# Performance work log

Hardware: AMD Instinct MI355X
Metric: run time of the kernel (lower is better)

Reference implementation:

```python
import jax, jax.numpy as jnp
import numpy as np
import math

H = 1024
E = 16
ENT_STRENGTH = 0.5
COHERENCE_TIME = 10.0
TIME_STEP = 0.0
K = 2
# static list of rotation pairs (i<j), applied sequentially as in the torch double loop
PAIRS = np.array([(i, j) for i in range(E) for j in range(i + 1, E)], dtype=np.int32)


def _mlp(x, w1, b1, w2, b2):
    h = jax.nn.gelu(x @ w1 + b1, approximate=False)  # torch default GELU = exact erf
    return h @ w2 + b2


def _apply_entanglement(amps, ent):
    # sequential Givens rotations over expert pairs; carry shape [B,S,E]
    pairs = jnp.asarray(PAIRS)

    def step(carry, pair):
        i, j = pair[0], pair[1]
        angle = ent[i, j] * ENT_STRENGTH
        c, s = jnp.cos(angle), jnp.sin(angle)
        ai = jnp.take(carry, i, axis=-1)  # [B,S]
        aj = jnp.take(carry, j, axis=-1)
        oh_i = jax.nn.one_hot(i, E, dtype=carry.dtype)
        oh_j = jax.nn.one_hot(j, E, dtype=carry.dtype)
        new = (carry * (1.0 - oh_i - oh_j)
               + (c * ai - s * aj)[..., None] * oh_i
               + (s * ai + c * aj)[..., None] * oh_j)
        return new, None

    out, _ = jax.lax.scan(step, amps, pairs)
    return out


def setup_inputs() -> dict:
    key = jax.random.key(0)
    ks = jax.random.split(key, 10)
    sc1 = 1.0 / math.sqrt(H)
    sc2 = 1.0 / math.sqrt(H // 2)
    return {
        "hidden_states": jax.random.normal(ks[0], (4, 4096, H), dtype=jnp.float32),
        "w1a": jax.random.uniform(ks[1], (H, H // 2), jnp.float32, -sc1, sc1),
        "b1a": jnp.zeros((H // 2,), jnp.float32),
        "w2a": jax.random.uniform(ks[2], (H // 2, E), jnp.float32, -sc2, sc2),
        "b2a": jnp.zeros((E,), jnp.float32),
        "w1p": jax.random.uniform(ks[3], (H, H // 2), jnp.float32, -sc1, sc1),
        "b1p": jnp.zeros((H // 2,), jnp.float32),
        "w2p": jax.random.uniform(ks[4], (H // 2, E), jnp.float32, -sc2, sc2),
        "b2p": jnp.zeros((E,), jnp.float32),
        "ent": jax.random.normal(ks[5], (E, E), dtype=jnp.float32) * 0.1,
    }


def reference(hidden_states, w1a, b1a, w2a, b2a, w1p, b1p, w2p, b2p, ent):
    raw_amps = _mlp(hidden_states, w1a, b1a, w2a, b2a)                 # [B,S,E]
    raw_phases = jnp.tanh(_mlp(hidden_states, w1p, b1p, w2p, b2p)) * jnp.float32(math.pi)
    amplitudes = jnp.sqrt(jax.nn.softmax(jnp.abs(raw_amps), axis=-1))
    entangled = _apply_entanglement(amplitudes, ent)
    coherence = jnp.exp(jnp.float32(-TIME_STEP / COHERENCE_TIME))      # time_step buffer = 0 -> 1.0
    decoherent = entangled * coherence
    probs = decoherent ** 2
    probs = probs / jnp.maximum(jnp.sum(jnp.abs(probs), axis=-1, keepdims=True), 1e-12)
    top_p, top_i = jax.lax.top_k(probs, K)
    top_p = top_p / jnp.maximum(jnp.sum(jnp.abs(top_p), axis=-1, keepdims=True), 1e-12)
    return top_p, top_i, decoherent, raw_phases, probs
```

## Files before the change

### kernel.cpp

```cpp
#include <hip/hip_runtime.h>
#include <math.h>

#define NTOK   16384
#define HDIM   1024
#define HHALF  512
#define NE     16

#define OFF_TP  0
#define OFF_TI  (NTOK * 2)
#define OFF_DEC (NTOK * 4)
#define OFF_PH  (OFF_DEC + NTOK * NE)
#define OFF_PR  (OFF_PH + NTOK * NE)

typedef _Float16 half8 __attribute__((ext_vector_type(8)));
typedef _Float16 half4 __attribute__((ext_vector_type(4)));
typedef float f32x16 __attribute__((ext_vector_type(16)));
typedef float f32x4 __attribute__((ext_vector_type(4)));

#define LO_SCALE     2048.0f
#define LO_SCALE_INV (1.0f / 2048.0f)
#define MFMA32(a,b,c) __builtin_amdgcn_mfma_f32_32x32x16_f16(a,b,c,0,0,0)
#define MFMA16(a,b,c) __builtin_amdgcn_mfma_f32_16x16x32_f16(a,b,c,0,0,0)

#define BAR() asm volatile("s_waitcnt lgkmcnt(0)\n\ts_barrier" ::: "memory")

__device__ __forceinline__ float gelu_exact(float x) {
    return 0.5f * x * (1.0f + erff(x * 0.70710678118654752440f));
}

__device__ __forceinline__ void cvt_split(float4 v, half4& hi, half4& lo) {
    _Float16 h0 = (_Float16)v.x, h1 = (_Float16)v.y,
             h2 = (_Float16)v.z, h3 = (_Float16)v.w;
    hi = (half4){h0, h1, h2, h3};
    lo = (half4){(_Float16)((v.x - (float)h0) * LO_SCALE),
                 (_Float16)((v.y - (float)h1) * LO_SCALE),
                 (_Float16)((v.z - (float)h2) * LO_SCALE),
                 (_Float16)((v.w - (float)h3) * LO_SCALE)};
}

__global__ void __launch_bounds__(256)
qir_wtrans(const float* __restrict__ w1a, const float* __restrict__ w1p,
           _Float16* __restrict__ wt, float* __restrict__ out)
{
    int u = blockIdx.x * 256 + threadIdx.x;
    out[OFF_PH + u] = 0.0f;
    out[OFF_PH + 262144 + u] = 0.0f;

    int l  = u & 63;
    int f  = (u >> 6) & 7;
    int sl = (u >> 9) & 7;
    int kc = (u >> 12) & 31;
    int ph = u >> 17;
    int nf = f >> 2, kh = (f >> 1) & 1, pl = f & 1;
    int col = sl * 64 + nf * 32 + (l & 31);
    int k0  = kc * 32 + kh * 16 + (l >> 5) * 8;
    const float* __restrict__ W = ph ? w1p : w1a;
    half8 v;
    #pragma unroll
    for (int j = 0; j < 8; ++j) {
        float x = W[(size_t)(k0 + j) * HHALF + col];
        _Float16 h = (_Float16)x;
        v[j] = pl ? (_Float16)((x - (float)h) * LO_SCALE) : h;
    }
    *(half8*)&wt[(size_t)u * 8] = v;
}

__device__ __forceinline__ void kstep(
    int kc, const float* __restrict__ aptr, const _Float16* __restrict__ bptr,
    char* Acur, char* Anxt, int a_rd, int a_off0, int a_off1,
    half8 (&Bc)[8], half8 (&Bn)[8],
    float4 (&xw)[2], float4 (&xl)[2],
    f32x16& a00, f32x16& a01, f32x16& a10, f32x16& a11,
    f32x16& c00, f32x16& c01, f32x16& c10, f32x16& c11)
{
    if (kc + 2 < 32) {
        xl[0] = *(const float4*)(aptr + (kc + 2) * 32);
        xl[1] = *(const float4*)(aptr + (kc + 2) * 32 + 16);
    }
    if (kc + 1 < 32) {
        #pragma unroll
        for (int f = 0; f < 8; ++f)
            Bn[f] = *(const half8*)(bptr + (size_t)(kc + 1) * 32768 + f * 512);
    }
    #pragma unroll
    for (int kh = 0; kh < 2; ++kh) {
        const char* Ah = Acur + kh * 4096 + a_rd;
        half8 ah0 = *(const half8*)(Ah);
        half8 ah1 = *(const half8*)(Ah + 512);
        half8 al0 = *(const half8*)(Ah + 8192);
        half8 al1 = *(const half8*)(Ah + 8192 + 512);
        half8 bh0 = Bc[kh * 2],     bl0 = Bc[kh * 2 + 1];
        half8 bh1 = Bc[4 + kh * 2], bl1 = Bc[4 + kh * 2 + 1];
        a00 = MFMA32(ah0, bh0, a00); c00 = MFMA32(al0, bh0, c00); c00 = MFMA32(ah0, bl0, c00);
        a01 = MFMA32(ah0, bh1, a01); c01 = MFMA32(al0, bh1, c01); c01 = MFMA32(ah0, bl1, c01);
        a10 = MFMA32(ah1, bh0, a10); c10 = MFMA32(al1, bh0, c10); c10 = MFMA32(ah1, bl0, c10);
        a11 = MFMA32(ah1, bh1, a11); c11 = MFMA32(al1, bh1, c11); c11 = MFMA32(ah1, bl1, c11);
    }
    if (kc + 1 < 32) {
        half4 hv, lv;
        cvt_split(xw[0], hv, lv);
        *(half4*)(Anxt + a_off0) = hv; *(half4*)(Anxt + a_off0 + 8192) = lv;
        cvt_split(xw[1], hv, lv);
        *(half4*)(Anxt + a_off1) = hv; *(half4*)(Anxt + a_off1 + 8192) = lv;
    }
    BAR();
}

__global__ void __launch_bounds__(512, 2)
qir_gemm(const float* __restrict__ xg, const _Float16* __restrict__ wt,
         const float* __restrict__ b1a, const float* __restrict__ w2a, const float* __restrict__ b2a,
         const float* __restrict__ b1p, const float* __restrict__ w2p, const float* __restrict__ b2p,
         float* __restrict__ out)
{
    extern __shared__ char smem[];
    const int tid = threadIdx.x;
    const int l  = tid & 63;
    const int w  = tid >> 6;
    const int wm = w >> 2;
    const int wn = w & 3;
    const int bid  = blockIdx.x;
    const int mblk = bid & 127;
    const int v    = bid >> 7;
    const int ph   = v & 1;
    const int nh   = v >> 1;
    const int tok0 = mblk * 128;

    const float* __restrict__ b1 = ph ? b1p : b1a;
    const float* __restrict__ w2 = ph ? w2p : w2a;
    const float* __restrict__ b2 = ph ? b2p : b2a;
    const _Float16* __restrict__ wtp = wt + ((size_t)ph << 20);

    char* const Ab0 = smem;
    char* const Ab1 = smem + 16384;

    const int r  = tid >> 2;
    const int kq = tid & 3;
    const float* __restrict__ aptr = xg + (size_t)(tok0 + r) * HDIM + kq * 4;
    const int a_off0 = (kq >> 1) * 2048 + r * 16 + (kq & 1) * 8;
    const int a_off1 = a_off0 + 4096;
    const int a_rd = (l >> 5) * 2048 + (wm * 64 + (l & 31)) * 16;

    const _Float16* __restrict__ bptr = wtp + (nh * 4 + wn) * 4096 + (size_t)l * 8;

    f32x16 a00{}, a01{}, a10{}, a11{}, c00{}, c01{}, c10{}, c11{};
    #pragma unroll
    for (int rg = 0; rg < 16; ++rg) {
        a00[rg] = 0.f; a01[rg] = 0.f; a10[rg] = 0.f; a11[rg] = 0.f;
        c00[rg] = 0.f; c01[rg] = 0.f; c10[rg] = 0.f; c11[rg] = 0.f;
    }

    half8 Bc[8], Bn[8];
    float4 xw[2], xl[2];

    {
        float4 v0 = *(const float4*)(aptr);
        float4 v1 = *(const float4*)(aptr + 16);
        half4 hv, lv;
        cvt_split(v0, hv, lv);
        *(half4*)(Ab0 + a_off0) = hv; *(half4*)(Ab0 + a_off0 + 8192) = lv;
        cvt_split(v1, hv, lv);
        *(half4*)(Ab0 + a_off1) = hv; *(half4*)(Ab0 + a_off1 + 8192) = lv;
    }
    #pragma unroll
    for (int f = 0; f < 8; ++f) Bc[f] = *(const half8*)(bptr + f * 512);
    xw[0] = *(const float4*)(aptr + 32);
    xw[1] = *(const float4*)(aptr + 48);
    BAR();

    for (int kk = 0; kk < 16; ++kk) {
        kstep(2 * kk,     aptr, bptr, Ab0, Ab1, a_rd, a_off0, a_off1,
              Bc, Bn, xw, xl, a00, a01, a10, a11, c00, c01, c10, c11);
        kstep(2 * kk + 1, aptr, bptr, Ab1, Ab0, a_rd, a_off0, a_off1,
              Bn, Bc, xl, xw, a00, a01, a10, a11, c00, c01, c10, c11);
    }

    const int col0 = nh * 256 + wn * 64 + (l & 31);
    const float bb0 = b1[col0], bb1 = b1[col0 + 32];
    #pragma unroll
    for (int rg = 0; rg < 16; ++rg) {
        a00[rg] = gelu_exact(a00[rg] + c00[rg] * LO_SCALE_INV + bb0);
        a01[rg] = gelu_exact(a01[rg] + c01[rg] * LO_SCALE_INV + bb1);
        a10[rg] = gelu_exact(a10[rg] + c10[rg] * LO_SCALE_INV + bb0);
        a11[rg] = gelu_exact(a11[rg] + c11[rg] * LO_SCALE_INV + bb1);
    }

    char* const Hw = smem + w * 4096;
    char* const hb = Hw + ((l >> 3) & 3) * 1024 + (l & 7) * 2;
    float* const P = (float*)(smem + 32768);

    half8 w2h[2], w2l[2];
    #pragma unroll
    for (int nf = 0; nf < 2; ++nf) {
        #pragma unroll
        for (int j = 0; j < 8; ++j) {
            int kg = nh * 256 + wn * 64 + nf * 32 + (l >> 4) * 8 + j;
            float vv = w2[(size_t)kg * NE + (l & 15)];
            _Float16 hh = (_Float16)vv;
            w2h[nf][j] = hh;
            w2l[nf][j] = (_Float16)((vv - (float)hh) * LO_SCALE);
        }
    }

    f32x4 acc2[4], acc2s[4];
    #pragma unroll
    for (int m16 = 0; m16 < 4; ++m16)
        #pragma unroll
        for (int rg = 0; rg < 4; ++rg) { acc2[m16][rg] = 0.f; acc2s[m16][rg] = 0.f; }

#define H2PASS(ACC0, ACC1, NF, PL)                                             \
    {                                                                          \
        _Pragma("unroll")                                                      \
        for (int rg = 0; rg < 16; ++rg) {                                      \
            int row0 = (rg & 3) + 8 * (rg >> 2) + 4 * (l >> 5);                \
            { float vv = ACC0[rg]; _Float16 hh = (_Float16)vv;                 \
              *(_Float16*)(hb + row0 * 16) =                                   \
                  (PL) ? (_Float16)(vv - (float)hh) : hh; }                    \
            { float vv = ACC1[rg]; _Float16 hh = (_Float16)vv;                 \
              *(_Float16*)(hb + (32 + row0) * 16) =                            \
                  (PL) ? (_Float16)(vv - (float)hh) : hh; }                    \
        }                                                                      \
        _Pragma("unroll")                                                      \
        for (int m16 = 0; m16 < 4; ++m16) {                                    \
            half8 a2 = *(const half8*)(Hw + (l >> 4) * 1024 +                  \
                                       (m16 * 16 + (l & 15)) * 16);            \
            acc2[m16] = MFMA16(a2, w2h[NF], acc2[m16]);                        \
            if (!(PL)) acc2s[m16] = MFMA16(a2, w2l[NF], acc2s[m16]);           \
        }                                                                      \
    }

    H2PASS(a00, a10, 0, 0)
    H2PASS(a01, a11, 1, 0)
    H2PASS(a00, a10, 0, 1)
    H2PASS(a01, a11, 1, 1)
#undef H2PASS

    #pragma unroll
    for (int m16 = 0; m16 < 4; ++m16)
        #pragma unroll
        for (int rg = 0; rg < 4; ++rg) {
            int row = m16 * 16 + ((l >> 4) << 2) + rg;
            P[w * 1024 + row * 16 + (l & 15)] =
                acc2[m16][rg] + acc2s[m16][rg] * LO_SCALE_INV;
        }
    __syncthreads();

    #pragma unroll
    for (int rep = 0; rep < 4; ++rep) {
        int oi = tid + rep * 512;
        int t = oi >> 4, e = oi & 15;
        int bw = (t >> 6) * 4, tl = t & 63;
        float sum = 0.5f * b2[e]
                  + P[(bw + 0) * 1024 + tl * 16 + e]
                  + P[(bw + 1) * 1024 + tl * 16 + e]
                  + P[(bw + 2) * 1024 + tl * 16 + e]
                  + P[(bw + 3) * 1024 + tl * 16 + e];
        atomicAdd(out + (ph ? OFF_PH : OFF_PR) + (size_t)(tok0 + t) * NE + e, sum);
    }
}

__global__ void __launch_bounds__(512)
qir_mlp(const float* __restrict__ xg,
        const float* __restrict__ w1a, const float* __restrict__ b1a,
        const float* __restrict__ w2a, const float* __restrict__ b2a,
        const float* __restrict__ w1p, const float* __restrict__ b1p,
        const float* __restrict__ w2p, const float* __restrict__ b2p,
        float* __restrict__ out)
{
    __shared__ float sh_w[16][HHALF];
    __shared__ float sh_x[16][68];

    const int tid  = threadIdx.x;
    const int cg   = tid & 63;
    const int tg   = tid >> 6;
    const int tok0 = blockIdx.x * 64;
    const int cA   = cg * 4;
    const int cB   = 256 + cg * 4;

    for (int phase = 0; phase < 2; ++phase) {
        const float* __restrict__ w1 = phase ? w1p : w1a;
        const float* __restrict__ b1 = phase ? b1p : b1a;
        const float* __restrict__ w2 = phase ? w2p : w2a;
        const float* __restrict__ b2 = phase ? b2p : b2a;

        float acc[8][8];
        #pragma unroll
        for (int t = 0; t < 8; ++t)
            #pragma unroll
            for (int c = 0; c < 8; ++c) acc[t][c] = 0.0f;

        float4 wreg[4];
        float4 xreg = make_float4(0.f, 0.f, 0.f, 0.f);

        auto load_chunk = [&](int kc) {
            #pragma unroll
            for (int p = 0; p < 4; ++p) {
                int f  = tid + p * 512;
                int k  = f >> 7;
                int c4 = (f & 127) << 2;
                wreg[p] = *(const float4*)&w1[(kc * 16 + k) * HHALF + c4];
            }
            if (tid < 256) {
                int t  = tid >> 2;
                int k4 = (tid & 3) << 2;
                xreg = *(const float4*)&xg[(size_t)(tok0 + t) * HDIM + kc * 16 + k4];
            }
        };

        load_chunk(0);
        for (int kc = 0; kc < HDIM / 16; ++kc) {
            __syncthreads();
            #pragma unroll
            for (int p = 0; p < 4; ++p) {
                int f  = tid + p * 512;
                int k  = f >> 7;
                int c4 = (f & 127) << 2;
                *(float4*)&sh_w[k][c4] = wreg[p];
            }
            if (tid < 256) {
                int t  = tid >> 2;
                int k4 = (tid & 3) << 2;
                sh_x[k4 + 0][t] = xreg.x;
                sh_x[k4 + 1][t] = xreg.y;
                sh_x[k4 + 2][t] = xreg.z;
                sh_x[k4 + 3][t] = xreg.w;
            }
            __syncthreads();
            if (kc + 1 < HDIM / 16) load_chunk(kc + 1);

            #pragma unroll 4
            for (int k = 0; k < 16; ++k) {
                float4 xa = *(const float4*)&sh_x[k][tg * 8];
                float4 xb = *(const float4*)&sh_x[k][tg * 8 + 4];
                float4 wa = *(const float4*)&sh_w[k][cA];
                float4 wb = *(const float4*)&sh_w[k][cB];
                float xs[8] = {xa.x, xa.y, xa.z, xa.w, xb.x, xb.y, xb.z, xb.w};
                float ws[8] = {wa.x, wa.y, wa.z, wa.w, wb.x, wb.y, wb.z, wb.w};
                #pragma unroll
                for (int t = 0; t < 8; ++t)
                    #pragma unroll
                    for (int c = 0; c < 8; ++c)
                        acc[t][c] = fmaf(xs[t], ws[c], acc[t][c]);
            }
        }

        {
            float4 bA4 = *(const float4*)&b1[cA];
            float4 bB4 = *(const float4*)&b1[cB];
            float bs[8] = {bA4.x, bA4.y, bA4.z, bA4.w, bB4.x, bB4.y, bB4.z, bB4.w};
            #pragma unroll
            for (int t = 0; t < 8; ++t)
                #pragma unroll
                for (int c = 0; c < 8; ++c)
                    acc[t][c] = gelu_exact(acc[t][c] + bs[c]);
        }

        for (int e = 0; e < NE; ++e) {
            float w2v[8];
            #pragma unroll
            for (int j = 0; j < 4; ++j) {
                w2v[j]     = w2[(cA + j) * NE + e];
                w2v[4 + j] = w2[(cB + j) * NE + e];
            }
            float bias2 = b2[e];
            #pragma unroll
            for (int t = 0; t < 8; ++t) {
                float s = 0.0f;
                #pragma unroll
                for (int j = 0; j < 8; ++j) s = fmaf(acc[t][j], w2v[j], s);
                #pragma unroll
                for (int off = 1; off < 64; off <<= 1)
                    s += __shfl_xor(s, off, 64);
                if (cg == 0) {
                    float raw   = s + bias2;
                    int   token = tok0 + tg * 8 + t;
                    out[(phase ? OFF_PH : OFF_PR) + (size_t)token * NE + e] = raw;
                }
            }
        }
    }
}

__global__ void __launch_bounds__(256)
qir_epilogue(const float* __restrict__ ent, float* __restrict__ out)
{
    __shared__ float sh_c[120], sh_s[120];
    const int tid = threadIdx.x;
    if (tid < 120) {
        int rem = tid, i = 0;
        while (rem >= 15 - i) { rem -= 15 - i; ++i; }
        int j = i + 1 + rem;
        float ang = ent[i * NE + j] * 0.5f;
        sh_c[tid] = cosf(ang);
        sh_s[tid] = sinf(ang);
    }
    __syncthreads();

    const int token = blockIdx.x * 256 + tid;

    #pragma unroll
    for (int q = 0; q < 4; ++q) {
        float4 v = *(const float4*)&out[OFF_PH + (size_t)token * NE + q * 4];
        v.x = tanhf(v.x) * 3.14159265358979323846f;
        v.y = tanhf(v.y) * 3.14159265358979323846f;
        v.z = tanhf(v.z) * 3.14159265358979323846f;
        v.w = tanhf(v.w) * 3.14159265358979323846f;
        *(float4*)&out[OFF_PH + (size_t)token * NE + q * 4] = v;
    }

    float a[16];
    #pragma unroll
    for (int q = 0; q < 4; ++q) {
        float4 v = *(const float4*)&out[OFF_PR + (size_t)token * NE + q * 4];
        a[q*4+0] = v.x; a[q*4+1] = v.y; a[q*4+2] = v.z; a[q*4+3] = v.w;
    }

    float m = fabsf(a[0]);
    #pragma unroll
    for (int e = 1; e < 16; ++e) m = fmaxf(m, fabsf(a[e]));
    float ssum = 0.0f;
    #pragma unroll
    for (int e = 0; e < 16; ++e) { a[e] = expf(fabsf(a[e]) - m); ssum += a[e]; }
    float inv = 1.0f / ssum;
    #pragma unroll
    for (int e = 0; e < 16; ++e) a[e] = sqrtf(a[e] * inv);

    {
        int p = 0;
        #pragma unroll
        for (int i = 0; i < 16; ++i) {
            #pragma unroll
            for (int j = i + 1; j < 16; ++j) {
                float c = sh_c[p], s = sh_s[p]; ++p;
                float ai = a[i], aj = a[j];
                a[i] = c * ai - s * aj;
                a[j] = s * ai + c * aj;
            }
        }
    }

    #pragma unroll
    for (int q = 0; q < 4; ++q)
        *(float4*)&out[OFF_DEC + (size_t)token * NE + q * 4] =
            make_float4(a[q*4], a[q*4+1], a[q*4+2], a[q*4+3]);

    float pr[16];
    float s2 = 0.0f;
    #pragma unroll
    for (int e = 0; e < 16; ++e) { pr[e] = a[e] * a[e]; s2 += pr[e]; }
    float inv2 = 1.0f / fmaxf(s2, 1e-12f);
    #pragma unroll
    for (int e = 0; e < 16; ++e) pr[e] *= inv2;
    #pragma unroll
    for (int q = 0; q < 4; ++q)
        *(float4*)&out[OFF_PR + (size_t)token * NE + q * 4] =
            make_float4(pr[q*4], pr[q*4+1], pr[q*4+2], pr[q*4+3]);

    float bv = pr[0]; int bi = 0;
    #pragma unroll
    for (int e = 1; e < 16; ++e) if (pr[e] > bv) { bv = pr[e]; bi = e; }
    float sv = -1.0f; int si = 0;
    #pragma unroll
    for (int e = 0; e < 16; ++e) if (e != bi && pr[e] > sv) { sv = pr[e]; si = e; }
    float ts = fmaxf(fabsf(bv) + fabsf(sv), 1e-12f);
    out[OFF_TP + (size_t)token * 2 + 0] = bv / ts;
    out[OFF_TP + (size_t)token * 2 + 1] = sv / ts;
    out[OFF_TI + (size_t)token * 2 + 0] = (float)bi;
    out[OFF_TI + (size_t)token * 2 + 1] = (float)si;
}

extern "C" void kernel_launch(void* const* d_in, const int* in_sizes, int n_in,
                              void* d_out, int out_size, void* d_ws, size_t ws_size,
                              hipStream_t stream) {
    const float* xg  = (const float*)d_in[0];
    const float* w1a = (const float*)d_in[1];
    const float* b1a = (const float*)d_in[2];
    const float* w2a = (const float*)d_in[3];
    const float* b2a = (const float*)d_in[4];
    const float* w1p = (const float*)d_in[5];
    const float* b1p = (const float*)d_in[6];
    const float* w2p = (const float*)d_in[7];
    const float* b2p = (const float*)d_in[8];
    const float* ent = (const float*)d_in[9];
    float* out = (float*)d_out;

    if (ws_size >= (size_t)4 * 1024 * 1024) {
        _Float16* wt = (_Float16*)d_ws;
        qir_wtrans<<<1024, 256, 0, stream>>>(w1a, w1p, wt, out);
        qir_gemm<<<512, 512, 65536, stream>>>(xg, wt, b1a, w2a, b2a,
                                              b1p, w2p, b2p, out);
    } else {
        qir_mlp<<<NTOK / 64, 512, 0, stream>>>(xg, w1a, b1a, w2a, b2a,
                                               w1p, b1p, w2p, b2p, out);
    }
    qir_epilogue<<<NTOK / 256, 256, 0, stream>>>(ent, out);
}
```

Baseline: 131.7 us.

## Remap GEMM warps to 128x32 strips sharing B fragments across four M tiles

Changes the per-wave tile of the first GEMM from 64x64 (2x2 of 32x32 MFMA tiles) to 128x32 (4x1), so each wave loads half as much B weight data per k-step but reads twice as much A from LDS. The second-layer projection is reorganized to match: hidden activations are staged per wave in padded LDS rows, and partial sums from all 8 waves are reduced instead of 4. This trades global B traffic and registers for more LDS reads and a larger cross-wave reduction.

```diff
diff --git a/kernel.cpp b/kernel.cpp
--- a/kernel.cpp
+++ b/kernel.cpp
@@ -68,10 +68,9 @@
 __device__ __forceinline__ void kstep(
     int kc, const float* __restrict__ aptr, const _Float16* __restrict__ bptr,
     char* Acur, char* Anxt, int a_rd, int a_off0, int a_off1,
-    half8 (&Bc)[8], half8 (&Bn)[8],
+    half8 (&Bc)[4], half8 (&Bn)[4],
     float4 (&xw)[2], float4 (&xl)[2],
-    f32x16& a00, f32x16& a01, f32x16& a10, f32x16& a11,
-    f32x16& c00, f32x16& c01, f32x16& c10, f32x16& c11)
+    f32x16 (&am)[4], f32x16 (&cm)[4])
 {
     if (kc + 2 < 32) {
         xl[0] = *(const float4*)(aptr + (kc + 2) * 32);
@@ -79,22 +78,25 @@
     }
     if (kc + 1 < 32) {
         #pragma unroll
-        for (int f = 0; f < 8; ++f)
-            Bn[f] = *(const half8*)(bptr + (size_t)(kc + 1) * 32768 + f * 512);
+        for (int j = 0; j < 4; ++j)
+            Bn[j] = *(const half8*)(bptr + (size_t)(kc + 1) * 32768 + j * 512);
     }
     #pragma unroll
     for (int kh = 0; kh < 2; ++kh) {
         const char* Ah = Acur + kh * 4096 + a_rd;
-        half8 ah0 = *(const half8*)(Ah);
-        half8 ah1 = *(const half8*)(Ah + 512);
-        half8 al0 = *(const half8*)(Ah + 8192);
-        half8 al1 = *(const half8*)(Ah + 8192 + 512);
-        half8 bh0 = Bc[kh * 2],     bl0 = Bc[kh * 2 + 1];
-        half8 bh1 = Bc[4 + kh * 2], bl1 = Bc[4 + kh * 2 + 1];
-        a00 = MFMA32(ah0, bh0, a00); c00 = MFMA32(al0, bh0, c00); c00 = MFMA32(ah0, bl0, c00);
-        a01 = MFMA32(ah0, bh1, a01); c01 = MFMA32(al0, bh1, c01); c01 = MFMA32(ah0, bl1, c01);
-        a10 = MFMA32(ah1, bh0, a10); c10 = MFMA32(al1, bh0, c10); c10 = MFMA32(ah1, bl0, c10);
-        a11 = MFMA32(ah1, bh1, a11); c11 = MFMA32(al1, bh1, c11); c11 = MFMA32(ah1, bl1, c11);
+        half8 ah[4], al[4];
+        #pragma unroll
+        for (int mf = 0; mf < 4; ++mf) {
+            ah[mf] = *(const half8*)(Ah + mf * 512);
+            al[mf] = *(const half8*)(Ah + 8192 + mf * 512);
+        }
+        half8 bh = Bc[kh * 2], bl = Bc[kh * 2 + 1];
+        #pragma unroll
+        for (int mf = 0; mf < 4; ++mf) {
+            am[mf] = MFMA32(ah[mf], bh, am[mf]);
+            cm[mf] = MFMA32(al[mf], bh, cm[mf]);
+            cm[mf] = MFMA32(ah[mf], bl, cm[mf]);
+        }
     }
     if (kc + 1 < 32) {
         half4 hv, lv;
@@ -116,8 +118,6 @@
     const int tid = threadIdx.x;
     const int l  = tid & 63;
     const int w  = tid >> 6;
-    const int wm = w >> 2;
-    const int wn = w & 3;
     const int bid  = blockIdx.x;
     const int mblk = bid & 127;
     const int v    = bid >> 7;
@@ -138,18 +138,19 @@
     const float* __restrict__ aptr = xg + (size_t)(tok0 + r) * HDIM + kq * 4;
     const int a_off0 = (kq >> 1) * 2048 + r * 16 + (kq & 1) * 8;
     const int a_off1 = a_off0 + 4096;
-    const int a_rd = (l >> 5) * 2048 + (wm * 64 + (l & 31)) * 16;
-
-    const _Float16* __restrict__ bptr = wtp + (nh * 4 + wn) * 4096 + (size_t)l * 8;
-
-    f32x16 a00{}, a01{}, a10{}, a11{}, c00{}, c01{}, c10{}, c11{};
-    #pragma unroll
-    for (int rg = 0; rg < 16; ++rg) {
-        a00[rg] = 0.f; a01[rg] = 0.f; a10[rg] = 0.f; a11[rg] = 0.f;
-        c00[rg] = 0.f; c01[rg] = 0.f; c10[rg] = 0.f; c11[rg] = 0.f;
-    }
-
-    half8 Bc[8], Bn[8];
+    const int a_rd = (l >> 5) * 2048 + (l & 31) * 16;
+
+    const int c32 = nh * 8 + w;
+    const _Float16* __restrict__ bptr =
+        wtp + (c32 >> 1) * 4096 + (c32 & 1) * 2048 + (size_t)l * 8;
+
+    f32x16 am[4], cm[4];
+    #pragma unroll
+    for (int mf = 0; mf < 4; ++mf)
+        #pragma unroll
+        for (int rg = 0; rg < 16; ++rg) { am[mf][rg] = 0.f; cm[mf][rg] = 0.f; }
+
+    half8 Bc[4], Bn[4];
     float4 xw[2], xl[2];
 
     {
@@ -162,98 +163,98 @@
         *(half4*)(Ab0 + a_off1) = hv; *(half4*)(Ab0 + a_off1 + 8192) = lv;
     }
     #pragma unroll
-    for (int f = 0; f < 8; ++f) Bc[f] = *(const half8*)(bptr + f * 512);
+    for (int j = 0; j < 4; ++j) Bc[j] = *(const half8*)(bptr + j * 512);
     xw[0] = *(const float4*)(aptr + 32);
     xw[1] = *(const float4*)(aptr + 48);
     BAR();
 
     for (int kk = 0; kk < 16; ++kk) {
         kstep(2 * kk,     aptr, bptr, Ab0, Ab1, a_rd, a_off0, a_off1,
-              Bc, Bn, xw, xl, a00, a01, a10, a11, c00, c01, c10, c11);
+              Bc, Bn, xw, xl, am, cm);
         kstep(2 * kk + 1, aptr, bptr, Ab1, Ab0, a_rd, a_off0, a_off1,
-              Bn, Bc, xl, xw, a00, a01, a10, a11, c00, c01, c10, c11);
-    }
-
-    const int col0 = nh * 256 + wn * 64 + (l & 31);
-    const float bb0 = b1[col0], bb1 = b1[col0 + 32];
-    #pragma unroll
-    for (int rg = 0; rg < 16; ++rg) {
-        a00[rg] = gelu_exact(a00[rg] + c00[rg] * LO_SCALE_INV + bb0);
-        a01[rg] = gelu_exact(a01[rg] + c01[rg] * LO_SCALE_INV + bb1);
-        a10[rg] = gelu_exact(a10[rg] + c10[rg] * LO_SCALE_INV + bb0);
-        a11[rg] = gelu_exact(a11[rg] + c11[rg] * LO_SCALE_INV + bb1);
-    }
-
-    char* const Hw = smem + w * 4096;
-    char* const hb = Hw + ((l >> 3) & 3) * 1024 + (l & 7) * 2;
-    float* const P = (float*)(smem + 32768);
-
-    half8 w2h[2], w2l[2];
-    #pragma unroll
-    for (int nf = 0; nf < 2; ++nf) {
-        #pragma unroll
-        for (int j = 0; j < 8; ++j) {
-            int kg = nh * 256 + wn * 64 + nf * 32 + (l >> 4) * 8 + j;
-            float vv = w2[(size_t)kg * NE + (l & 15)];
-            _Float16 hh = (_Float16)vv;
-            w2h[nf][j] = hh;
-            w2l[nf][j] = (_Float16)((vv - (float)hh) * LO_SCALE);
-        }
-    }
-
-    f32x4 acc2[4], acc2s[4];
-    #pragma unroll
-    for (int m16 = 0; m16 < 4; ++m16)
-        #pragma unroll
-        for (int rg = 0; rg < 4; ++rg) { acc2[m16][rg] = 0.f; acc2s[m16][rg] = 0.f; }
-
-#define H2PASS(ACC0, ACC1, NF, PL)                                             \
-    {                                                                          \
-        _Pragma("unroll")                                                      \
-        for (int rg = 0; rg < 16; ++rg) {                                      \
-            int row0 = (rg & 3) + 8 * (rg >> 2) + 4 * (l >> 5);                \
-            { float vv = ACC0[rg]; _Float16 hh = (_Float16)vv;                 \
-              *(_Float16*)(hb + row0 * 16) =                                   \
-                  (PL) ? (_Float16)(vv - (float)hh) : hh; }                    \
-            { float vv = ACC1[rg]; _Float16 hh = (_Float16)vv;                 \
-              *(_Float16*)(hb + (32 + row0) * 16) =                            \
-                  (PL) ? (_Float16)(vv - (float)hh) : hh; }                    \
-        }                                                                      \
-        _Pragma("unroll")                                                      \
-        for (int m16 = 0; m16 < 4; ++m16) {                                    \
-            half8 a2 = *(const half8*)(Hw + (l >> 4) * 1024 +                  \
-                                       (m16 * 16 + (l & 15)) * 16);            \
-            acc2[m16] = MFMA16(a2, w2h[NF], acc2[m16]);                        \
-            if (!(PL)) acc2s[m16] = MFMA16(a2, w2l[NF], acc2s[m16]);           \
-        }                                                                      \
-    }
-
-    H2PASS(a00, a10, 0, 0)
-    H2PASS(a01, a11, 1, 0)
-    H2PASS(a00, a10, 0, 1)
-    H2PASS(a01, a11, 1, 1)
-#undef H2PASS
-
-    #pragma unroll
-    for (int m16 = 0; m16 < 4; ++m16)
-        #pragma unroll
-        for (int rg = 0; rg < 4; ++rg) {
-            int row = m16 * 16 + ((l >> 4) << 2) + rg;
-            P[w * 1024 + row * 16 + (l & 15)] =
-                acc2[m16][rg] + acc2s[m16][rg] * LO_SCALE_INV;
-        }
+              Bn, Bc, xl, xw, am, cm);
+    }
+
+    const float bb = b1[nh * 256 + w * 32 + (l & 31)];
+    #pragma unroll
+    for (int mf = 0; mf < 4; ++mf)
+        #pragma unroll
+        for (int rg = 0; rg < 16; ++rg)
+            am[mf][rg] = gelu_exact(am[mf][rg] + cm[mf][rg] * LO_SCALE_INV + bb);
+
+    char* const Hw = smem + w * 5120;
+
+    half8 w2h, w2l;
+    #pragma unroll
+    for (int j = 0; j < 8; ++j) {
+        int kg = nh * 256 + w * 32 + (l >> 4) * 8 + j;
+        float vv = w2[(size_t)kg * NE + (l & 15)];
+        _Float16 hh = (_Float16)vv;
+        w2h[j] = hh;
+        w2l[j] = (_Float16)((vv - (float)hh) * LO_SCALE);
+    }
+
+    f32x4 acc2[2][4], acc2s[2][4];
+    #pragma unroll
+    for (int p2 = 0; p2 < 2; ++p2)
+        #pragma unroll
+        for (int m16 = 0; m16 < 4; ++m16)
+            #pragma unroll
+            for (int rg = 0; rg < 4; ++rg) { acc2[p2][m16][rg] = 0.f; acc2s[p2][m16][rg] = 0.f; }
+
+    #pragma unroll
+    for (int p2 = 0; p2 < 2; ++p2) {
+        #pragma unroll
+        for (int fr = 0; fr < 2; ++fr)
+            #pragma unroll
+            for (int rg = 0; rg < 16; ++rg) {
+                int row = fr * 32 + (rg & 3) + 8 * (rg >> 2) + 4 * (l >> 5);
+                float vv = am[p2 * 2 + fr][rg];
+                *(_Float16*)(Hw + row * 80 + (l & 31) * 2) = (_Float16)vv;
+            }
+        #pragma unroll
+        for (int m16 = 0; m16 < 4; ++m16) {
+            half8 a2 = *(const half8*)(Hw + (m16 * 16 + (l & 15)) * 80 + (l >> 4) * 16);
+            acc2[p2][m16]  = MFMA16(a2, w2h, acc2[p2][m16]);
+            acc2s[p2][m16] = MFMA16(a2, w2l, acc2s[p2][m16]);
+        }
+        #pragma unroll
+        for (int fr = 0; fr < 2; ++fr)
+            #pragma unroll
+            for (int rg = 0; rg < 16; ++rg) {
+                int row = fr * 32 + (rg & 3) + 8 * (rg >> 2) + 4 * (l >> 5);
+                float vv = am[p2 * 2 + fr][rg];
+                _Float16 hh = (_Float16)vv;
+                *(_Float16*)(Hw + row * 80 + (l & 31) * 2) = (_Float16)(vv - (float)hh);
+            }
+        #pragma unroll
+        for (int m16 = 0; m16 < 4; ++m16) {
+            half8 a2 = *(const half8*)(Hw + (m16 * 16 + (l & 15)) * 80 + (l >> 4) * 16);
+            acc2[p2][m16] = MFMA16(a2, w2h, acc2[p2][m16]);
+        }
+    }
+
+    __syncthreads();
+    float* const P = (float*)smem;
+    #pragma unroll
+    for (int p2 = 0; p2 < 2; ++p2)
+        #pragma unroll
+        for (int m16 = 0; m16 < 4; ++m16)
+            #pragma unroll
+            for (int rg = 0; rg < 4; ++rg) {
+                int t = p2 * 64 + m16 * 16 + ((l >> 4) << 2) + rg;
+                P[w * 2048 + t * 16 + (l & 15)] =
+                    acc2[p2][m16][rg] + acc2s[p2][m16][rg] * LO_SCALE_INV;
+            }
     __syncthreads();
 
     #pragma unroll
     for (int rep = 0; rep < 4; ++rep) {
         int oi = tid + rep * 512;
         int t = oi >> 4, e = oi & 15;
-        int bw = (t >> 6) * 4, tl = t & 63;
-        float sum = 0.5f * b2[e]
-                  + P[(bw + 0) * 1024 + tl * 16 + e]
-                  + P[(bw + 1) * 1024 + tl * 16 + e]
-                  + P[(bw + 2) * 1024 + tl * 16 + e]
-                  + P[(bw + 3) * 1024 + tl * 16 + e];
+        float sum = 0.5f * b2[e];
+        #pragma unroll
+        for (int w8 = 0; w8 < 8; ++w8) sum += P[w8 * 2048 + t * 16 + e];
         atomicAdd(out + (ph ? OFF_PH : OFF_PR) + (size_t)(tok0 + t) * NE + e, sum);
     }
 }
```

Result: faster. 120.8 us (-8.3%).

## Process two K-chunks per barrier with larger LDS double buffer

Applied to the files above, without the earlier changes.

Restructures the main GEMM K loop so that each iteration stages a 64-wide K slab of the activations in LDS instead of a 32-wide one. This halves the number of block-wide barriers. The B fragments for the second half-slab are prefetched into a separate register set, and the next slab's B loads are issued in the middle of the MFMA sequence to overlap global latency with compute. In exchange, the A double buffer grows to 64 KB of LDS and the register footprint rises. The LDS growth could limit the two-blocks-per-CU occupancy and needs a matching dynamic shared-memory size at launch.

```diff
diff --git a/kernel.cpp b/kernel.cpp
--- a/kernel.cpp
+++ b/kernel.cpp
@@ -63,47 +63,6 @@
         v[j] = pl ? (_Float16)((x - (float)h) * LO_SCALE) : h;
     }
     *(half8*)&wt[(size_t)u * 8] = v;
-}
-
-__device__ __forceinline__ void kstep(
-    int kc, const float* __restrict__ aptr, const _Float16* __restrict__ bptr,
-    char* Acur, char* Anxt, int a_rd, int a_off0, int a_off1,
-    half8 (&Bc)[8], half8 (&Bn)[8],
-    float4 (&xw)[2], float4 (&xl)[2],
-    f32x16& a00, f32x16& a01, f32x16& a10, f32x16& a11,
-    f32x16& c00, f32x16& c01, f32x16& c10, f32x16& c11)
-{
-    if (kc + 2 < 32) {
-        xl[0] = *(const float4*)(aptr + (kc + 2) * 32);
-        xl[1] = *(const float4*)(aptr + (kc + 2) * 32 + 16);
-    }
-    if (kc + 1 < 32) {
-        #pragma unroll
-        for (int f = 0; f < 8; ++f)
-            Bn[f] = *(const half8*)(bptr + (size_t)(kc + 1) * 32768 + f * 512);
-    }
-    #pragma unroll
-    for (int kh = 0; kh < 2; ++kh) {
-        const char* Ah = Acur + kh * 4096 + a_rd;
-        half8 ah0 = *(const half8*)(Ah);
-        half8 ah1 = *(const half8*)(Ah + 512);
-        half8 al0 = *(const half8*)(Ah + 8192);
-        half8 al1 = *(const half8*)(Ah + 8192 + 512);
-        half8 bh0 = Bc[kh * 2],     bl0 = Bc[kh * 2 + 1];
-        half8 bh1 = Bc[4 + kh * 2], bl1 = Bc[4 + kh * 2 + 1];
-        a00 = MFMA32(ah0, bh0, a00); c00 = MFMA32(al0, bh0, c00); c00 = MFMA32(ah0, bl0, c00);
-        a01 = MFMA32(ah0, bh1, a01); c01 = MFMA32(al0, bh1, c01); c01 = MFMA32(ah0, bl1, c01);
-        a10 = MFMA32(ah1, bh0, a10); c10 = MFMA32(al1, bh0, c10); c10 = MFMA32(ah1, bl0, c10);
-        a11 = MFMA32(ah1, bh1, a11); c11 = MFMA32(al1, bh1, c11); c11 = MFMA32(ah1, bl1, c11);
-    }
-    if (kc + 1 < 32) {
-        half4 hv, lv;
-        cvt_split(xw[0], hv, lv);
-        *(half4*)(Anxt + a_off0) = hv; *(half4*)(Anxt + a_off0 + 8192) = lv;
-        cvt_split(xw[1], hv, lv);
-        *(half4*)(Anxt + a_off1) = hv; *(half4*)(Anxt + a_off1 + 8192) = lv;
-    }
-    BAR();
 }
 
 __global__ void __launch_bounds__(512, 2)
@@ -130,14 +89,10 @@
     const float* __restrict__ b2 = ph ? b2p : b2a;
     const _Float16* __restrict__ wtp = wt + ((size_t)ph << 20);
 
-    char* const Ab0 = smem;
-    char* const Ab1 = smem + 16384;
-
     const int r  = tid >> 2;
     const int kq = tid & 3;
     const float* __restrict__ aptr = xg + (size_t)(tok0 + r) * HDIM + kq * 4;
-    const int a_off0 = (kq >> 1) * 2048 + r * 16 + (kq & 1) * 8;
-    const int a_off1 = a_off0 + 4096;
+    const int a_woff = (kq >> 1) * 2048 + r * 16 + (kq & 1) * 8;
     const int a_rd = (l >> 5) * 2048 + (wm * 64 + (l & 31)) * 16;
 
     const _Float16* __restrict__ bptr = wtp + (nh * 4 + wn) * 4096 + (size_t)l * 8;
@@ -149,29 +104,84 @@
         c00[rg] = 0.f; c01[rg] = 0.f; c10[rg] = 0.f; c11[rg] = 0.f;
     }
 
-    half8 Bc[8], Bn[8];
-    float4 xw[2], xl[2];
+    half8 Bc[8], Bd[8];
+    float4 xw[4];
 
     {
-        float4 v0 = *(const float4*)(aptr);
-        float4 v1 = *(const float4*)(aptr + 16);
-        half4 hv, lv;
-        cvt_split(v0, hv, lv);
-        *(half4*)(Ab0 + a_off0) = hv; *(half4*)(Ab0 + a_off0 + 8192) = lv;
-        cvt_split(v1, hv, lv);
-        *(half4*)(Ab0 + a_off1) = hv; *(half4*)(Ab0 + a_off1 + 8192) = lv;
+        #pragma unroll
+        for (int c = 0; c < 4; ++c) {
+            float4 vv = *(const float4*)(aptr + c * 16);
+            half4 hv, lv;
+            cvt_split(vv, hv, lv);
+            *(half4*)(smem + a_woff + c * 4096) = hv;
+            *(half4*)(smem + a_woff + c * 4096 + 16384) = lv;
+        }
     }
     #pragma unroll
     for (int f = 0; f < 8; ++f) Bc[f] = *(const half8*)(bptr + f * 512);
-    xw[0] = *(const float4*)(aptr + 32);
-    xw[1] = *(const float4*)(aptr + 48);
     BAR();
 
-    for (int kk = 0; kk < 16; ++kk) {
-        kstep(2 * kk,     aptr, bptr, Ab0, Ab1, a_rd, a_off0, a_off1,
-              Bc, Bn, xw, xl, a00, a01, a10, a11, c00, c01, c10, c11);
-        kstep(2 * kk + 1, aptr, bptr, Ab1, Ab0, a_rd, a_off0, a_off1,
-              Bn, Bc, xl, xw, a00, a01, a10, a11, c00, c01, c10, c11);
+    #pragma unroll 1
+    for (int p = 0; p < 16; ++p) {
+        char* const cur = smem + (p & 1) * 32768;
+        char* const nxt = smem + ((p & 1) ^ 1) * 32768;
+
+        #pragma unroll
+        for (int f = 0; f < 8; ++f)
+            Bd[f] = *(const half8*)(bptr + (size_t)(2 * p + 1) * 32768 + f * 512);
+        if (p + 1 < 16) {
+            #pragma unroll
+            for (int c = 0; c < 4; ++c)
+                xw[c] = *(const float4*)(aptr + (p + 1) * 64 + c * 16);
+        }
+
+        #pragma unroll
+        for (int j = 0; j < 2; ++j) {
+            const char* Aj = cur + j * 4096 + a_rd;
+            half8 ah0 = *(const half8*)(Aj);
+            half8 ah1 = *(const half8*)(Aj + 512);
+            half8 al0 = *(const half8*)(Aj + 16384);
+            half8 al1 = *(const half8*)(Aj + 16384 + 512);
+            half8 bh0 = Bc[j * 2],     bl0 = Bc[j * 2 + 1];
+            half8 bh1 = Bc[4 + j * 2], bl1 = Bc[4 + j * 2 + 1];
+            a00 = MFMA32(ah0, bh0, a00); c00 = MFMA32(al0, bh0, c00); c00 = MFMA32(ah0, bl0, c00);
+            a01 = MFMA32(ah0, bh1, a01); c01 = MFMA32(al0, bh1, c01); c01 = MFMA32(ah0, bl1, c01);
+            a10 = MFMA32(ah1, bh0, a10); c10 = MFMA32(al1, bh0, c10); c10 = MFMA32(ah1, bl0, c10);
+            a11 = MFMA32(ah1, bh1, a11); c11 = MFMA32(al1, bh1, c11); c11 = MFMA32(ah1, bl1, c11);
+        }
+
+        if (p + 1 < 16) {
+            #pragma unroll
+            for (int f = 0; f < 8; ++f)
+                Bc[f] = *(const half8*)(bptr + (size_t)(2 * p + 2) * 32768 + f * 512);
+        }
+
+        #pragma unroll
+        for (int j = 2; j < 4; ++j) {
+            const char* Aj = cur + j * 4096 + a_rd;
+            half8 ah0 = *(const half8*)(Aj);
+            half8 ah1 = *(const half8*)(Aj + 512);
+            half8 al0 = *(const half8*)(Aj + 16384);
+            half8 al1 = *(const half8*)(Aj + 16384 + 512);
+            const int kh = j - 2;
+            half8 bh0 = Bd[kh * 2],     bl0 = Bd[kh * 2 + 1];
+            half8 bh1 = Bd[4 + kh * 2], bl1 = Bd[4 + kh * 2 + 1];
+            a00 = MFMA32(ah0, bh0, a00); c00 = MFMA32(al0, bh0, c00); c00 = MFMA32(ah0, bl0, c00);
+            a01 = MFMA32(ah0, bh1, a01); c01 = MFMA32(al0, bh1, c01); c01 = MFMA32(ah0, bl1, c01);
+            a10 = MFMA32(ah1, bh0, a10); c10 = MFMA32(al1, bh0, c10); c10 = MFMA32(ah1, bl0, c10);
+            a11 = MFMA32(ah1, bh1, a11); c11 = MFMA32(al1, bh1, c11); c11 = MFMA32(ah1, bl1, c11);
+        }
+
+        if (p + 1 < 16) {
+            #pragma unroll
+            for (int c = 0; c < 4; ++c) {
+                half4 hv, lv;
+                cvt_split(xw[c], hv, lv);
+                *(half4*)(nxt + a_woff + c * 4096) = hv;
+                *(half4*)(nxt + a_woff + c * 4096 + 16384) = lv;
+            }
+        }
+        BAR();
     }
 
     const int col0 = nh * 256 + wn * 64 + (l & 31);
```

Result: slower. 136.5 us (+3.6%).
